# Performance work log

Measured on AMD Instinct MI355X. Metric: run time of the kernel, lower is better.

The kernel has to match this reference:

```python
import jax, jax.numpy as jnp
import numpy as np

S, B, C = 7, 2, 20
L_COORD, L_NOOBJ = 5.0, 0.5
BATCH = 16384


def setup_inputs() -> dict:
    key = jax.random.key(0)
    k1, k2, k3 = jax.random.split(key, 3)
    pred = jax.random.normal(k1, (BATCH, S, S, 5 * B + C), dtype=jnp.float32)
    target = jax.random.uniform(k2, (BATCH, S, S, 5 * B + C), dtype=jnp.float32)
    conf = target[..., 4]
    target = target.at[..., 4].set(jnp.where(conf > 0.9, conf, 0.0))
    # per-cell branch choice (replaces python random.random() > 0.5 per object)
    choice = jax.random.randint(k3, (BATCH, S, S), 0, 2, dtype=jnp.int32)
    return {"pred": pred, "target": target, "choice": choice}


def reference(pred, target, choice):
    dt = pred.dtype
    tconf = target[..., 4]
    obj = tconf > 0                      # [B,S,S]
    m = obj.astype(dt)
    n_obj = jnp.maximum(m.sum(), 1.0)
    c = choice.astype(bool)              # True -> box 1, False -> box 2
    cE = c[..., None]

    pxy = jnp.where(cE, pred[..., 0:2], pred[..., 5:7])
    pwh = jnp.where(cE, pred[..., 2:4], pred[..., 7:9])
    txy = jnp.where(cE, target[..., 0:2], target[..., 5:7])
    twh = jnp.where(cE, target[..., 2:4], target[..., 7:9])
    twh = jnp.where(obj[..., None], twh, 1.0)  # sqrt-safe outside obj mask
    pobj = jnp.where(c, pred[..., 4], pred[..., 9])
    tobj = jnp.where(c, tconf, target[..., 9])

    # per-object: mean over 2 elems for xy and for (wh - sqrt(twh)), summed over objects
    loc_cell = ((pxy - txy) ** 2).mean(-1) + ((pwh - jnp.sqrt(twh)) ** 2).mean(-1)
    loc_loss = L_COORD * (m * loc_cell).sum()
    obj_loss = (m * (pobj - tobj) ** 2).sum()

    nm = (tconf == 0).astype(dt)
    n_no = jnp.maximum(nm.sum(), 1.0)
    noobj_loss = L_NOOBJ * (
        (nm * (pred[..., 4] - tconf) ** 2).sum() / n_no
        + (nm * (pred[..., 9] - target[..., 9]) ** 2).sum() / n_no
    )

    # faithful to original: softmax applied BEFORE CrossEntropyLoss (double softmax)
    logits = pred[..., 5 * B:5 * B + C]
    sm = jax.nn.softmax(logits, axis=-1)
    logp = jax.nn.log_softmax(sm, axis=-1)
    tcls = jnp.argmax(target[..., 5 * B:5 * B + C], axis=-1)
    ce = -jnp.take_along_axis(logp, tcls[..., None], axis=-1)[..., 0]
    cls_loss = (m * ce).sum() / n_obj

    return (loc_loss, cls_loss, obj_loss, noobj_loss)
```

## Files before the change

### kernel.cpp

```cpp
#include <hip/hip_runtime.h>
#include <math.h>


typedef float vf4 __attribute__((ext_vector_type(4)));

constexpr int NCH = 30;
constexpr int CC  = 20;
constexpr int ROW = 8;
constexpr int T   = 256;
constexpr int CPB = 128;
constexpr int NF4 = CPB * NCH * 2 / 4;
constexpr int HF4 = NF4 / 2;
constexpr int GRID = 1280;

__device__ __forceinline__ void issue_chunk(
    const float* __restrict__ pred, const float* __restrict__ target,
    const int* __restrict__ choice, int cc, int ncells, int tid,
    vf4 (&r)[8], int& ci)
{
    long long base = (long long)cc * CPB;
    if (base + CPB <= (long long)ncells) {
        const vf4* Pb = (const vf4*)(pred + base * NCH);
        const vf4* Tb = (const vf4*)(target + base * NCH);
        #pragma unroll
        for (int j = 0; j < 8; ++j) {
            int k = j * T + tid;
            if (k < NF4)
                r[j] = (k < HF4) ? __builtin_nontemporal_load(&Pb[k])
                                 : __builtin_nontemporal_load(&Tb[k - HF4]);
        }
    } else {
        int nfl = (int)(ncells - base) * NCH;
        const float* Pf = pred + base * NCH;
        const float* Tf = target + base * NCH;
        #pragma unroll
        for (int j = 0; j < 8; ++j) {
            int k = j * T + tid;
            vf4 v = (vf4)(0.f, 0.f, 0.f, 0.f);
            if (k < NF4) {
                int kk = (k < HF4) ? k : k - HF4;
                const float* src = (k < HF4) ? Pf : Tf;
                int b = 4 * kk;
                if (b + 0 < nfl) v.x = src[b + 0];
                if (b + 1 < nfl) v.y = src[b + 1];
                if (b + 2 < nfl) v.z = src[b + 2];
                if (b + 3 < nfl) v.w = src[b + 3];
            }
            r[j] = v;
        }
    }
    if (tid < CPB) {
        long long ce = base + tid;
        ci = (ce < (long long)ncells) ? __builtin_nontemporal_load(&choice[ce]) : 0;
    }
}

__global__ __launch_bounds__(T) void yolo_main(
    const float* __restrict__ pred, const float* __restrict__ target,
    const int* __restrict__ choice, float* __restrict__ ws,
    int ncells, int nchunks)
{
    __shared__ float sbuf[2 * CPB * NCH];
    const int tid = threadIdx.x;

    float a_loc = 0.f, a_ce = 0.f, a_obj = 0.f, a_no = 0.f;
    float a_nob = 0.f, a_nno = 0.f;

    vf4 r[8];
    int ci = 0;
    int c = blockIdx.x;
    if (c < nchunks) issue_chunk(pred, target, choice, c, ncells, tid, r, ci);

    for (; c < nchunks; c += GRID) {
        __syncthreads();
        #pragma unroll
        for (int j = 0; j < 8; ++j) {
            int k = j * T + tid;
            if (k < NF4) *(vf4*)&sbuf[k * 4] = r[j];
        }
        int myc = ci;
        __syncthreads();

        int cn = c + GRID;
        if (cn < nchunks) issue_chunk(pred, target, choice, cn, ncells, tid, r, ci);

        if (tid < CPB && (long long)c * CPB + tid < ncells) {
            const float* sp  = &sbuf[tid * NCH];
            const float* stt = &sbuf[CPB * NCH + tid * NCH];
            float p[NCH], t[NCH];
            #pragma unroll
            for (int i = 0; i < NCH / 2; ++i) {
                float2 v = *(const float2*)&sp[2 * i];  p[2*i] = v.x; p[2*i+1] = v.y;
            }
            #pragma unroll
            for (int i = 0; i < NCH / 2; ++i) {
                float2 w = *(const float2*)&stt[2 * i]; t[2*i] = w.x; t[2*i+1] = w.y;
            }
            bool csel = myc != 0;

            float tconf = t[4];
            bool  obj = tconf > 0.0f;
            float m = obj ? 1.0f : 0.0f;

            float pxy0 = csel ? p[0] : p[5];
            float pxy1 = csel ? p[1] : p[6];
            float pwh0 = csel ? p[2] : p[7];
            float pwh1 = csel ? p[3] : p[8];
            float pobj = csel ? p[4] : p[9];
            float txy0 = csel ? t[0] : t[5];
            float txy1 = csel ? t[1] : t[6];
            float twh0 = csel ? t[2] : t[7];
            float twh1 = csel ? t[3] : t[8];
            if (!obj) { twh0 = 1.0f; twh1 = 1.0f; }
            float tobj = csel ? tconf : t[9];

            float dx = pxy0 - txy0, dy = pxy1 - txy1;
            float dw = pwh0 - sqrtf(twh0), dh = pwh1 - sqrtf(twh1);
            a_loc += m * (0.5f * (dx*dx + dy*dy) + 0.5f * (dw*dw + dh*dh));

            float dob = pobj - tobj;
            a_obj += m * dob * dob;

            float nm = (tconf == 0.0f) ? 1.0f : 0.0f;
            float d4 = p[4] - tconf, d9 = p[9] - t[9];
            a_no += nm * (d4 * d4 + d9 * d9);

            a_nob += m;
            a_nno += nm;

            int   tcls  = 0;
            float tbest = t[10];
            #pragma unroll
            for (int i = 1; i < CC; ++i) {
                float v = t[10 + i];
                if (v > tbest) { tbest = v; tcls = i; }
            }
            float mx = p[10];
            #pragma unroll
            for (int i = 1; i < CC; ++i) mx = fmaxf(mx, p[10 + i]);
            float e[CC];
            float Z = 0.f;
            #pragma unroll
            for (int i = 0; i < CC; ++i) { e[i] = __expf(p[10+i] - mx); Z += e[i]; }
            float rZ = 1.0f / Z;
            float Z2 = 0.f, sm_t = 0.f;
            #pragma unroll
            for (int i = 0; i < CC; ++i) {
                float sm = e[i] * rZ;
                Z2 += __expf(sm);
                if (i == tcls) sm_t = sm;
            }
            a_ce += m * (__logf(Z2) - sm_t);
        }
    }

    #pragma unroll
    for (int off = 32; off > 0; off >>= 1) {
        a_loc += __shfl_down(a_loc, off);
        a_ce  += __shfl_down(a_ce,  off);
        a_obj += __shfl_down(a_obj, off);
        a_no  += __shfl_down(a_no,  off);
        a_nob += __shfl_down(a_nob, off);
        a_nno += __shfl_down(a_nno, off);
    }

    __shared__ float red[4][6];
    int wave = tid >> 6;
    int lane = tid & 63;
    if (lane == 0) {
        red[wave][0] = a_loc; red[wave][1] = a_ce;  red[wave][2] = a_obj;
        red[wave][3] = a_no;  red[wave][4] = a_nob; red[wave][5] = a_nno;
    }
    __syncthreads();
    if (tid < 6) {
        float v = red[0][tid] + red[1][tid] + red[2][tid] + red[3][tid];
        ws[(size_t)blockIdx.x * ROW + tid] = v;
    }
}

__global__ __launch_bounds__(256) void yolo_reduce(
    const float* __restrict__ ws, float* __restrict__ out, int nb)
{
    float s[6] = {0.f, 0.f, 0.f, 0.f, 0.f, 0.f};
    for (int b = threadIdx.x; b < nb; b += 256) {
        #pragma unroll
        for (int j = 0; j < 6; ++j) s[j] += ws[(size_t)b * ROW + j];
    }
    #pragma unroll
    for (int off = 32; off > 0; off >>= 1) {
        #pragma unroll
        for (int j = 0; j < 6; ++j) s[j] += __shfl_down(s[j], off);
    }
    __shared__ float red[4][6];
    int wave = threadIdx.x >> 6;
    int lane = threadIdx.x & 63;
    if (lane == 0) {
        #pragma unroll
        for (int j = 0; j < 6; ++j) red[wave][j] = s[j];
    }
    __syncthreads();
    if (threadIdx.x == 0) {
        float t[6];
        #pragma unroll
        for (int j = 0; j < 6; ++j)
            t[j] = red[0][j] + red[1][j] + red[2][j] + red[3][j];
        out[0] = 5.0f * t[0];
        out[1] = t[1] / fmaxf(t[4], 1.0f);
        out[2] = t[2];
        out[3] = 0.5f * t[3] / fmaxf(t[5], 1.0f);
    }
}

extern "C" void kernel_launch(void* const* d_in, const int* in_sizes, int n_in,
                              void* d_out, int out_size, void* d_ws, size_t ws_size,
                              hipStream_t stream) {
    const float* pred   = (const float*)d_in[0];
    const float* target = (const float*)d_in[1];
    const int*   choice = (const int*)d_in[2];
    float* out = (float*)d_out;
    float* ws  = (float*)d_ws;

    int ncells  = in_sizes[2];
    int nchunks = (ncells + CPB - 1) / CPB;
    int grid    = GRID < nchunks ? GRID : nchunks;
    yolo_main<<<grid, T, 0, stream>>>(pred, target, choice, ws, ncells, nchunks);
    yolo_reduce<<<1, 256, 0, stream>>>(ws, out, grid);
}
```

Measured before the change: 193.4 us.

## Stream chunks into LDS with direct global-to-LDS loads and a double buffer

Replaces register-staged vector loads plus explicit LDS stores with global_load_lds 16-byte transfers straight into a double-buffered LDS area, choice values included. Two chunks are kept in flight and hand-tuned vmcnt waits release the older one. This drops the register round-trip and the store phase and deepens prefetch. The cost is doubled LDS use (about 61 KB per block), which may limit occupancy, and fragile hand-counted waitcnt values; tail chunks are handled by clamping addresses rather than zero-filling.

```diff
diff --git a/kernel.cpp b/kernel.cpp
--- a/kernel.cpp
+++ b/kernel.cpp
@@ -9,50 +9,54 @@
 constexpr int ROW = 8;
 constexpr int T   = 256;
 constexpr int CPB = 128;
-constexpr int NF4 = CPB * NCH * 2 / 4;
-constexpr int HF4 = NF4 / 2;
 constexpr int GRID = 1280;
 
-__device__ __forceinline__ void issue_chunk(
-    const float* __restrict__ pred, const float* __restrict__ target,
-    const int* __restrict__ choice, int cc, int ncells, int tid,
-    vf4 (&r)[8], int& ci)
+constexpr int DATA_B   = CPB * NCH * 4;
+constexpr int CHOICE_B = CPB * 4;
+constexpr int BUF_B    = 2 * DATA_B + CHOICE_B;
+constexpr int NSLOT    = (2 * DATA_B) / 1024;
+
+__device__ __forceinline__ void gl_lds16(const void* g, void* l) {
+    __builtin_amdgcn_global_load_lds(
+        (__attribute__((address_space(1))) void*)g,
+        (__attribute__((address_space(3))) void*)l, 16, 0, 0);
+}
+
+__device__ __forceinline__ void issue_group(
+    const char* __restrict__ predB, const char* __restrict__ targetB,
+    const char* __restrict__ choiceB, long long cc, long long ncells,
+    int tid, char* ldsbuf)
 {
-    long long base = (long long)cc * CPB;
-    if (base + CPB <= (long long)ncells) {
-        const vf4* Pb = (const vf4*)(pred + base * NCH);
-        const vf4* Tb = (const vf4*)(target + base * NCH);
-        #pragma unroll
-        for (int j = 0; j < 8; ++j) {
-            int k = j * T + tid;
-            if (k < NF4)
-                r[j] = (k < HF4) ? __builtin_nontemporal_load(&Pb[k])
-                                 : __builtin_nontemporal_load(&Tb[k - HF4]);
+    const int w = tid >> 6, l = tid & 63;
+    const long long cbyteA  = cc * (long long)DATA_B;
+    const long long cbyteC  = cc * (long long)CHOICE_B;
+    const long long nbytesA = ncells * (long long)(NCH * 4);
+    const long long nbytesC = ncells * 4ll;
+    #pragma unroll
+    for (int jj = 0; jj < 8; ++jj) {
+        int s = w + jj * 4;
+        if (s < NSLOT) {
+            int f = s * 1024 + l * 16;
+            const char* src;
+            long long off;
+            if (f < DATA_B) { off = cbyteA + f;            src = predB; }
+            else            { off = cbyteA + (f - DATA_B); src = targetB; }
+            if (off + 16 > nbytesA) off = nbytesA - 16;
+            gl_lds16(src + off, ldsbuf + f);
+        } else if (s == NSLOT) {
+            if (l < 32) {
+                long long off = cbyteC + (long long)l * 16;
+                if (off + 16 > nbytesC) off = nbytesC - 16;
+                gl_lds16(choiceB + off, ldsbuf + 2 * DATA_B + l * 16);
+            }
         }
-    } else {
-        int nfl = (int)(ncells - base) * NCH;
-        const float* Pf = pred + base * NCH;
-        const float* Tf = target + base * NCH;
-        #pragma unroll
-        for (int j = 0; j < 8; ++j) {
-            int k = j * T + tid;
-            vf4 v = (vf4)(0.f, 0.f, 0.f, 0.f);
-            if (k < NF4) {
-                int kk = (k < HF4) ? k : k - HF4;
-                const float* src = (k < HF4) ? Pf : Tf;
-                int b = 4 * kk;
-                if (b + 0 < nfl) v.x = src[b + 0];
-                if (b + 1 < nfl) v.y = src[b + 1];
-                if (b + 2 < nfl) v.z = src[b + 2];
-                if (b + 3 < nfl) v.w = src[b + 3];
-            }
-            r[j] = v;
-        }
-    }
-    if (tid < CPB) {
-        long long ce = base + tid;
-        ci = (ce < (long long)ncells) ? __builtin_nontemporal_load(&choice[ce]) : 0;
-    }
+    }
+}
+
+__device__ __forceinline__ void wait_newer(int w, bool has_next) {
+    if (!has_next) { asm volatile("s_waitcnt vmcnt(0)" ::: "memory"); return; }
+    if (w == 3) asm volatile("s_waitcnt vmcnt(7)" ::: "memory");
+    else        asm volatile("s_waitcnt vmcnt(8)" ::: "memory");
 }
 
 __global__ __launch_bounds__(T) void yolo_main(
@@ -60,41 +64,45 @@
     const int* __restrict__ choice, float* __restrict__ ws,
     int ncells, int nchunks)
 {
-    __shared__ float sbuf[2 * CPB * NCH];
+    __shared__ __align__(16) char sbuf[2 * BUF_B];
+    __shared__ float red[4][6];
     const int tid = threadIdx.x;
+    const int w   = tid >> 6;
+
+    const char* predB   = (const char*)pred;
+    const char* targetB = (const char*)target;
+    const char* choiceB = (const char*)choice;
 
     float a_loc = 0.f, a_ce = 0.f, a_obj = 0.f, a_no = 0.f;
     float a_nob = 0.f, a_nno = 0.f;
 
-    vf4 r[8];
-    int ci = 0;
-    int c = blockIdx.x;
-    if (c < nchunks) issue_chunk(pred, target, choice, c, ncells, tid, r, ci);
+    long long c = blockIdx.x;
+    int p = 0;
+    if (c < nchunks) {
+        issue_group(predB, targetB, choiceB, c, ncells, tid, sbuf);
+        if (c + GRID < nchunks)
+            issue_group(predB, targetB, choiceB, c + GRID, ncells, tid, sbuf + BUF_B);
+    }
 
     for (; c < nchunks; c += GRID) {
-        __syncthreads();
-        #pragma unroll
-        for (int j = 0; j < 8; ++j) {
-            int k = j * T + tid;
-            if (k < NF4) *(vf4*)&sbuf[k * 4] = r[j];
-        }
-        int myc = ci;
-        __syncthreads();
-
-        int cn = c + GRID;
-        if (cn < nchunks) issue_chunk(pred, target, choice, cn, ncells, tid, r, ci);
-
-        if (tid < CPB && (long long)c * CPB + tid < ncells) {
-            const float* sp  = &sbuf[tid * NCH];
-            const float* stt = &sbuf[CPB * NCH + tid * NCH];
-            float p[NCH], t[NCH];
+        bool has_next = (c + GRID < nchunks);
+        wait_newer(w, has_next);
+        __builtin_amdgcn_s_barrier();
+        asm volatile("" ::: "memory");
+
+        if (tid < CPB && c * CPB + tid < (long long)ncells) {
+            const float* bp  = (const float*)(sbuf + p * BUF_B);
+            const float* sp  = bp + tid * NCH;
+            const float* stt = bp + (DATA_B / 4) + tid * NCH;
+            int myc = ((const int*)(sbuf + p * BUF_B + 2 * DATA_B))[tid];
+            float pv[NCH], t[NCH];
             #pragma unroll
             for (int i = 0; i < NCH / 2; ++i) {
-                float2 v = *(const float2*)&sp[2 * i];  p[2*i] = v.x; p[2*i+1] = v.y;
+                float2 v = *(const float2*)&sp[2 * i];  pv[2*i] = v.x; pv[2*i+1] = v.y;
             }
             #pragma unroll
             for (int i = 0; i < NCH / 2; ++i) {
-                float2 w = *(const float2*)&stt[2 * i]; t[2*i] = w.x; t[2*i+1] = w.y;
+                float2 u = *(const float2*)&stt[2 * i]; t[2*i] = u.x; t[2*i+1] = u.y;
             }
             bool csel = myc != 0;
 
@@ -102,11 +110,11 @@
             bool  obj = tconf > 0.0f;
             float m = obj ? 1.0f : 0.0f;
 
-            float pxy0 = csel ? p[0] : p[5];
-            float pxy1 = csel ? p[1] : p[6];
-            float pwh0 = csel ? p[2] : p[7];
-            float pwh1 = csel ? p[3] : p[8];
-            float pobj = csel ? p[4] : p[9];
+            float pxy0 = csel ? pv[0] : pv[5];
+            float pxy1 = csel ? pv[1] : pv[6];
+            float pwh0 = csel ? pv[2] : pv[7];
+            float pwh1 = csel ? pv[3] : pv[8];
+            float pobj = csel ? pv[4] : pv[9];
             float txy0 = csel ? t[0] : t[5];
             float txy1 = csel ? t[1] : t[6];
             float twh0 = csel ? t[2] : t[7];
@@ -122,7 +130,7 @@
             a_obj += m * dob * dob;
 
             float nm = (tconf == 0.0f) ? 1.0f : 0.0f;
-            float d4 = p[4] - tconf, d9 = p[9] - t[9];
+            float d4 = pv[4] - tconf, d9 = pv[9] - t[9];
             a_no += nm * (d4 * d4 + d9 * d9);
 
             a_nob += m;
@@ -135,13 +143,13 @@
                 float v = t[10 + i];
                 if (v > tbest) { tbest = v; tcls = i; }
             }
-            float mx = p[10];
-            #pragma unroll
-            for (int i = 1; i < CC; ++i) mx = fmaxf(mx, p[10 + i]);
+            float mx = pv[10];
+            #pragma unroll
+            for (int i = 1; i < CC; ++i) mx = fmaxf(mx, pv[10 + i]);
             float e[CC];
             float Z = 0.f;
             #pragma unroll
-            for (int i = 0; i < CC; ++i) { e[i] = __expf(p[10+i] - mx); Z += e[i]; }
+            for (int i = 0; i < CC; ++i) { e[i] = __expf(pv[10+i] - mx); Z += e[i]; }
             float rZ = 1.0f / Z;
             float Z2 = 0.f, sm_t = 0.f;
             #pragma unroll
@@ -152,6 +160,15 @@
             }
             a_ce += m * (__logf(Z2) - sm_t);
         }
+
+        asm volatile("" ::: "memory");
+        __builtin_amdgcn_s_barrier();
+        asm volatile("" ::: "memory");
+
+        if (c + 2 * (long long)GRID < nchunks)
+            issue_group(predB, targetB, choiceB, c + 2 * GRID, ncells, tid,
+                        sbuf + p * BUF_B);
+        p ^= 1;
     }
 
     #pragma unroll
@@ -164,12 +181,10 @@
         a_nno += __shfl_down(a_nno, off);
     }
 
-    __shared__ float red[4][6];
-    int wave = tid >> 6;
     int lane = tid & 63;
     if (lane == 0) {
-        red[wave][0] = a_loc; red[wave][1] = a_ce;  red[wave][2] = a_obj;
-        red[wave][3] = a_no;  red[wave][4] = a_nob; red[wave][5] = a_nno;
+        red[w][0] = a_loc; red[w][1] = a_ce;  red[w][2] = a_obj;
+        red[w][3] = a_no;  red[w][4] = a_nob; red[w][5] = a_nno;
     }
     __syncthreads();
     if (tid < 6) {
```

New measurement: 214.5 us. +10.9%, slower.

## Replace LDS-staged double-buffered loads with direct per-thread global loads

Applied to the files above, without the earlier changes.

Removes the shared-memory staging and register prefetch of the next chunk. Each thread now reads its own cell's 30 pred and 30 target floats as float2 loads straight from global memory, and blocks shrink to 128 threads. This drops the LDS traffic and barriers, and no longer leaves half the threads idle during compute. The cost is strided, uncoalesced float2 accesses (120-byte stride per lane) and the loss of the explicit prefetch overlap, so it relies on the caches to absorb the access pattern.

```diff
diff --git a/kernel.cpp b/kernel.cpp
--- a/kernel.cpp
+++ b/kernel.cpp
@@ -2,91 +2,28 @@
 #include <math.h>
 
 
-typedef float vf4 __attribute__((ext_vector_type(4)));
-
 constexpr int NCH = 30;
 constexpr int CC  = 20;
 constexpr int ROW = 8;
-constexpr int T   = 256;
+constexpr int T   = 128;
 constexpr int CPB = 128;
-constexpr int NF4 = CPB * NCH * 2 / 4;
-constexpr int HF4 = NF4 / 2;
 constexpr int GRID = 1280;
-
-__device__ __forceinline__ void issue_chunk(
-    const float* __restrict__ pred, const float* __restrict__ target,
-    const int* __restrict__ choice, int cc, int ncells, int tid,
-    vf4 (&r)[8], int& ci)
-{
-    long long base = (long long)cc * CPB;
-    if (base + CPB <= (long long)ncells) {
-        const vf4* Pb = (const vf4*)(pred + base * NCH);
-        const vf4* Tb = (const vf4*)(target + base * NCH);
-        #pragma unroll
-        for (int j = 0; j < 8; ++j) {
-            int k = j * T + tid;
-            if (k < NF4)
-                r[j] = (k < HF4) ? __builtin_nontemporal_load(&Pb[k])
-                                 : __builtin_nontemporal_load(&Tb[k - HF4]);
-        }
-    } else {
-        int nfl = (int)(ncells - base) * NCH;
-        const float* Pf = pred + base * NCH;
-        const float* Tf = target + base * NCH;
-        #pragma unroll
-        for (int j = 0; j < 8; ++j) {
-            int k = j * T + tid;
-            vf4 v = (vf4)(0.f, 0.f, 0.f, 0.f);
-            if (k < NF4) {
-                int kk = (k < HF4) ? k : k - HF4;
-                const float* src = (k < HF4) ? Pf : Tf;
-                int b = 4 * kk;
-                if (b + 0 < nfl) v.x = src[b + 0];
-                if (b + 1 < nfl) v.y = src[b + 1];
-                if (b + 2 < nfl) v.z = src[b + 2];
-                if (b + 3 < nfl) v.w = src[b + 3];
-            }
-            r[j] = v;
-        }
-    }
-    if (tid < CPB) {
-        long long ce = base + tid;
-        ci = (ce < (long long)ncells) ? __builtin_nontemporal_load(&choice[ce]) : 0;
-    }
-}
 
 __global__ __launch_bounds__(T) void yolo_main(
     const float* __restrict__ pred, const float* __restrict__ target,
     const int* __restrict__ choice, float* __restrict__ ws,
     int ncells, int nchunks)
 {
-    __shared__ float sbuf[2 * CPB * NCH];
     const int tid = threadIdx.x;
 
     float a_loc = 0.f, a_ce = 0.f, a_obj = 0.f, a_no = 0.f;
     float a_nob = 0.f, a_nno = 0.f;
 
-    vf4 r[8];
-    int ci = 0;
-    int c = blockIdx.x;
-    if (c < nchunks) issue_chunk(pred, target, choice, c, ncells, tid, r, ci);
-
-    for (; c < nchunks; c += GRID) {
-        __syncthreads();
-        #pragma unroll
-        for (int j = 0; j < 8; ++j) {
-            int k = j * T + tid;
-            if (k < NF4) *(vf4*)&sbuf[k * 4] = r[j];
-        }
-        int myc = ci;
-        __syncthreads();
-
-        int cn = c + GRID;
-        if (cn < nchunks) issue_chunk(pred, target, choice, cn, ncells, tid, r, ci);
-
-        if (tid < CPB && (long long)c * CPB + tid < ncells) {
-            const float* sp  = &sbuf[tid * NCH];
-            const float* stt = &sbuf[CPB * NCH + tid * NCH];
+    for (long long c = blockIdx.x; c < nchunks; c += GRID) {
+        long long cell = c * CPB + tid;
+        if (cell < (long long)ncells) {
+            const float* sp  = pred   + cell * NCH;
+            const float* stt = target + cell * NCH;
             float p[NCH], t[NCH];
             #pragma unroll
             for (int i = 0; i < NCH / 2; ++i) {
@@ -96,6 +33,7 @@
             for (int i = 0; i < NCH / 2; ++i) {
                 float2 w = *(const float2*)&stt[2 * i]; t[2*i] = w.x; t[2*i+1] = w.y;
             }
+            int myc = choice[cell];
             bool csel = myc != 0;
 
             float tconf = t[4];
@@ -167,6 +105,7 @@
     __shared__ float red[4][6];
     int wave = tid >> 6;
     int lane = tid & 63;
+    if (tid < 6) { red[2][tid] = 0.f; red[3][tid] = 0.f; }
     if (lane == 0) {
         red[wave][0] = a_loc; red[wave][1] = a_ce;  red[wave][2] = a_obj;
         red[wave][3] = a_no;  red[wave][4] = a_nob; red[wave][5] = a_nno;
```

New measurement: 216.6 us. +12.0%, slower.
